# Kernel optimization log

Hardware: AMD Instinct MI355X
Metric: run time of the kernel (lower is better)

The kernel has to match this reference:

```python
import jax, jax.numpy as jnp
import numpy as np

N = 100000  # nodes
E = 1600000  # edges
F_IN = 512
H = 128
C = 40
L = 8
ALPHA = 0.1
THETA = 0.5


def setup_inputs() -> dict:
    key = jax.random.key(0)
    ks = jax.random.split(key, 8)
    x = jax.random.normal(ks[0], (N, F_IN), dtype=jnp.float32)
    edge_index = jax.random.randint(ks[1], (2, E), 0, N, dtype=jnp.int32)
    edge_weight = jax.random.uniform(ks[2], (E,), dtype=jnp.float32)
    W0 = jax.random.normal(ks[3], (F_IN, H), dtype=jnp.float32) * 0.05
    b0 = jnp.zeros((H,), dtype=jnp.float32)
    convW = jax.random.normal(ks[4], (L, H, H), dtype=jnp.float32) * 0.05
    W1 = jax.random.normal(ks[5], (H, C), dtype=jnp.float32) * 0.05
    b1 = jnp.zeros((C,), dtype=jnp.float32)
    return {"x": x, "edge_index": edge_index, "edge_weight": edge_weight,
            "W0": W0, "b0": b0, "convW": convW, "W1": W1, "b1": b1}


def reference(x, edge_index, edge_weight, W0, b0, convW, W1, b1):
    # eval mode, dropout=0.0 -> dropout is identity
    src, dst = edge_index[0], edge_index[1]
    h = jnp.maximum(x @ W0 + b0, 0.0)  # [N, H]
    x0 = h  # initial residual
    # GCN2Conv beta per layer: log(theta/layer + 1), layer = 1..L
    betas = jnp.log(THETA / jnp.arange(1, L + 1, dtype=jnp.float32) + 1.0)

    def layer(h, inputs):
        W, beta = inputs  # W: [H, H]
        # sparse adjacency propagation: sum_j A_ij * h_j
        msgs = h[src] * edge_weight[:, None]  # [E, H]
        agg = jax.ops.segment_sum(msgs, dst, num_segments=N)  # [N, H]
        # initial residual mixing + identity mapping (shared_weights=True)
        out = (1.0 - ALPHA) * agg + ALPHA * x0
        out = (1.0 - beta) * out + beta * (out @ W)
        return jnp.maximum(out, 0.0), None

    h, _ = jax.lax.scan(layer, h, (convW, betas))
    logits = h @ W1 + b1  # [N, C]
    return jax.nn.log_softmax(logits, axis=-1)
```

## Files before the change

### kernel.cpp

```cpp
#include <hip/hip_runtime.h>
#include <hip/hip_bf16.h>
#include <cmath>

#define NN 100000
#define NE 1600000
#define FIN 512
#define HD 128
#define NC 40
#define NL 8
#define SCB 512

typedef __attribute__((ext_vector_type(8))) short bh8;
typedef __attribute__((ext_vector_type(4))) float f4;
typedef __attribute__((ext_vector_type(4))) unsigned int u4;
typedef __attribute__((ext_vector_type(2))) unsigned int u2;

__device__ __forceinline__ float bflo(unsigned p){ return __uint_as_float(p << 16); }
__device__ __forceinline__ float bfhi(unsigned p){ return __uint_as_float(p & 0xffff0000u); }
__device__ __forceinline__ unsigned short f2bf(float f){
  unsigned u = __float_as_uint(f);
  u += 0x7fffu + ((u >> 16) & 1u);
  return (unsigned short)(u >> 16);
}
__device__ __forceinline__ unsigned pack2(float a, float b){
  return (unsigned)f2bf(a) | ((unsigned)f2bf(b) << 16);
}

__global__ void k_deg(const int* __restrict__ dst, int* __restrict__ deg, int e){
  for (int i = blockIdx.x * blockDim.x + threadIdx.x; i < e; i += gridDim.x * blockDim.x)
    atomicAdd(&deg[dst[i]], 1);
}

__global__ void k_scan(const int* __restrict__ deg, int* __restrict__ offs,
                       int* __restrict__ cur, int n){
  __shared__ int wsum[16];
  __shared__ int carry;
  int t = threadIdx.x, lane = t & 63, wid = t >> 6;
  if (t == 0) carry = 0;
  __syncthreads();
  for (int base = 0; base < n; base += 1024){
    int idx = base + t;
    int v = (idx < n) ? deg[idx] : 0;
    int orig = v;
    #pragma unroll
    for (int off = 1; off < 64; off <<= 1){
      int u = __shfl_up(v, off);
      if (lane >= off) v += u;
    }
    if (lane == 63) wsum[wid] = v;
    __syncthreads();
    if (wid == 0){
      int s = (lane < 16) ? wsum[lane] : 0;
      #pragma unroll
      for (int off = 1; off < 16; off <<= 1){
        int u = __shfl_up(s, off);
        if (lane >= off) s += u;
      }
      if (lane < 16) wsum[lane] = s;
    }
    __syncthreads();
    int wexcl = (wid == 0) ? 0 : wsum[wid - 1];
    int excl = carry + wexcl + (v - orig);
    if (idx < n){ offs[idx] = excl; cur[idx] = excl; }
    int ctot = wsum[15];
    __syncthreads();
    if (t == 0) carry += ctot;
    __syncthreads();
  }
  if (t == 0) offs[n] = carry;
}

__global__ void k_twt(const float* __restrict__ in, unsigned short* __restrict__ out,
                      int K, int C, int Cpad){
  int total = Cpad * K;
  for (int i = blockIdx.x * blockDim.x + threadIdx.x; i < total; i += gridDim.x * blockDim.x){
    int c = i / K, k = i % K;
    float v = (c < C) ? in[(size_t)k * C + c] : 0.f;
    out[i] = f2bf(v);
  }
}

__global__ __launch_bounds__(256) void k_g0sc(const float* __restrict__ X,
                                              const unsigned short* __restrict__ Wt,
                                              const float* __restrict__ b0,
                                              unsigned* __restrict__ Ha,
                                              unsigned* __restrict__ Hb, int n,
                                              const int* __restrict__ src,
                                              const int* __restrict__ dst,
                                              const float* __restrict__ wgt,
                                              int* __restrict__ cur,
                                              u2* __restrict__ epk, int e){
  __shared__ __attribute__((aligned(16))) char lds[33792];
  if ((int)blockIdx.x < SCB){
    int stride = SCB * 256;
    int i = blockIdx.x * 256 + threadIdx.x;
    for (; i + 3 * stride < e; i += 4 * stride){
      int i0 = i, i1 = i + stride, i2 = i + 2 * stride, i3 = i + 3 * stride;
      int d0 = dst[i0], d1 = dst[i1], d2 = dst[i2], d3 = dst[i3];
      int p0 = atomicAdd(&cur[d0], 1);
      int p1 = atomicAdd(&cur[d1], 1);
      int p2 = atomicAdd(&cur[d2], 1);
      int p3 = atomicAdd(&cur[d3], 1);
      u2 v0 = { (unsigned)src[i0], __float_as_uint(wgt[i0]) };
      u2 v1 = { (unsigned)src[i1], __float_as_uint(wgt[i1]) };
      u2 v2 = { (unsigned)src[i2], __float_as_uint(wgt[i2]) };
      u2 v3 = { (unsigned)src[i3], __float_as_uint(wgt[i3]) };
      epk[p0] = v0; epk[p1] = v1; epk[p2] = v2; epk[p3] = v3;
    }
    for (; i < e; i += stride){
      int d = dst[i];
      int p = atomicAdd(&cur[d], 1);
      u2 v = { (unsigned)src[i], __float_as_uint(wgt[i]) };
      epk[p] = v;
    }
    return;
  }
  char* ldsA = lds;
  char* ldsW = lds + 8192;
  float* ldsO = (float*)lds;
  int t = threadIdx.x;
  int w = t >> 6, lane = t & 63;
  int rowBase = (blockIdx.x - SCB) * 64;
  f4 acc[8];
  #pragma unroll
  for (int i = 0; i < 8; i++) acc[i] = (f4)0.f;

  for (int kk = 0; kk < 8; kk++){
    #pragma unroll
    for (int iter = 0; iter < 2; iter++){
      int r = t / 8 + iter * 32;
      int kc = (t % 8) * 8;
      int grow = rowBase + r;
      float4 f0 = {0,0,0,0}, f1 = {0,0,0,0};
      if (grow < n){
        const float4* p = (const float4*)(X + (size_t)grow * FIN + kk * 64 + kc);
        f0 = p[0]; f1 = p[1];
      }
      u4 pv = { pack2(f0.x, f0.y), pack2(f0.z, f0.w), pack2(f1.x, f1.y), pack2(f1.z, f1.w) };
      *(u4*)(ldsA + r * 128 + ((kc * 2) ^ ((r & 7) << 4))) = pv;
    }
    #pragma unroll
    for (int iter = 0; iter < 4; iter++){
      int c = t / 8 + iter * 32;
      int kc = (t % 8) * 8;
      bh8 v = *(const bh8*)(Wt + (size_t)c * FIN + kk * 64 + kc);
      *(bh8*)(ldsW + c * 128 + ((kc * 2) ^ ((c & 7) << 4))) = v;
    }
    __syncthreads();
    int rowf = (w << 4) + (lane & 15);
    #pragma unroll
    for (int ks = 0; ks < 2; ks++){
      bh8 fa = *(const bh8*)(ldsA + rowf * 128 + ((ks * 64 + (lane >> 4) * 16) ^ ((rowf & 7) << 4)));
      #pragma unroll
      for (int ct = 0; ct < 8; ct++){
        int colf = (ct << 4) + (lane & 15);
        bh8 fb = *(const bh8*)(ldsW + colf * 128 + ((ks * 64 + (lane >> 4) * 16) ^ ((colf & 7) << 4)));
        acc[ct] = __builtin_amdgcn_mfma_f32_16x16x32_bf16(fa, fb, acc[ct], 0, 0, 0);
      }
    }
    __syncthreads();
  }
  #pragma unroll
  for (int ct = 0; ct < 8; ct++){
    int colf = (ct << 4) + (lane & 15);
    float bb = b0[colf];
    #pragma unroll
    for (int i = 0; i < 4; i++){
      int r = (w << 4) + ((lane >> 4) << 2) + i;
      float v = acc[ct][i] + bb;
      ldsO[r * 132 + colf] = v > 0.f ? v : 0.f;
    }
  }
  __syncthreads();
  #pragma unroll
  for (int iter = 0; iter < 4; iter++){
    int r = iter * 16 + t / 16;
    int c8 = (t % 16) * 8;
    int grow = rowBase + r;
    if (grow < n){
      float* p = &ldsO[r * 132 + c8];
      u4 pv = { pack2(p[0], p[1]), pack2(p[2], p[3]), pack2(p[4], p[5]), pack2(p[6], p[7]) };
      *(u4*)(Ha + (size_t)grow * 64 + (t % 16) * 4) = pv;
      *(u4*)(Hb + (size_t)grow * 64 + (t % 16) * 4) = pv;
    }
  }
}

__global__ __launch_bounds__(512) void k_layer(const unsigned* __restrict__ Hin,
                                               const unsigned* __restrict__ X0,
                                               const int* __restrict__ offs,
                                               const u2* __restrict__ epk,
                                               const unsigned short* __restrict__ Wt,
                                               float beta,
                                               unsigned* __restrict__ Hout, int n){
  __shared__ __attribute__((aligned(16))) char ldsA[16384];
  int t = threadIdx.x;
  int w = t >> 6, lane = t & 63;
  int q = lane >> 4, l16 = lane & 15;
  int quadId = (w << 2) + q;
  int rowBase = blockIdx.x * 64;

  #pragma unroll
  for (int rr = 0; rr < 2; rr++){
    int lr = (quadId << 1) + rr;
    int d = rowBase + lr;
    bool act = d < n;
    int e0 = act ? offs[d] : 0;
    int e1 = act ? offs[d + 1] : 0;
    float a0=0.f,a1=0.f,a2=0.f,a3=0.f,a4=0.f,a5=0.f,a6=0.f,a7=0.f;
    int e = e0;
    for (; e + 7 < e1; e += 8){
      #pragma unroll
      for (int j = 0; j < 8; j++){
        u2 pe = epk[e + j];
        float wf = __uint_as_float(pe.y);
        u4 r = *(const u4*)(Hin + (size_t)pe.x * 64 + l16 * 4);
        a0 += wf * bflo(r.x); a1 += wf * bfhi(r.x);
        a2 += wf * bflo(r.y); a3 += wf * bfhi(r.y);
        a4 += wf * bflo(r.z); a5 += wf * bfhi(r.z);
        a6 += wf * bflo(r.w); a7 += wf * bfhi(r.w);
      }
    }
    for (; e < e1; e++){
      u2 pe = epk[e];
      float wf = __uint_as_float(pe.y);
      u4 r = *(const u4*)(Hin + (size_t)pe.x * 64 + l16 * 4);
      a0 += wf * bflo(r.x); a1 += wf * bfhi(r.x);
      a2 += wf * bflo(r.y); a3 += wf * bfhi(r.y);
      a4 += wf * bflo(r.z); a5 += wf * bfhi(r.z);
      a6 += wf * bflo(r.w); a7 += wf * bfhi(r.w);
    }
    u4 ov = { 0u, 0u, 0u, 0u };
    if (act){
      u4 xp = *(const u4*)(X0 + (size_t)d * 64 + l16 * 4);
      float v0 = 0.9f*a0 + 0.1f*bflo(xp.x), v1 = 0.9f*a1 + 0.1f*bfhi(xp.x);
      float v2 = 0.9f*a2 + 0.1f*bflo(xp.y), v3 = 0.9f*a3 + 0.1f*bfhi(xp.y);
      float v4 = 0.9f*a4 + 0.1f*bflo(xp.z), v5 = 0.9f*a5 + 0.1f*bfhi(xp.z);
      float v6 = 0.9f*a6 + 0.1f*bflo(xp.w), v7 = 0.9f*a7 + 0.1f*bfhi(xp.w);
      ov = (u4){ pack2(v0,v1), pack2(v2,v3), pack2(v4,v5), pack2(v6,v7) };
    }
    *(u4*)(ldsA + lr * 256 + ((l16 * 16) ^ ((lr & 7) << 4))) = ov;
  }
  __syncthreads();

  f4 acc[4];
  #pragma unroll
  for (int i = 0; i < 4; i++) acc[i] = (f4)0.f;
  int rowf = ((w & 3) << 4) + l16;
  int colBase = (w >> 2) << 6;
  #pragma unroll
  for (int ks = 0; ks < 4; ks++){
    bh8 fa = *(const bh8*)(ldsA + rowf * 256 + ((ks * 64 + q * 16) ^ ((rowf & 7) << 4)));
    #pragma unroll
    for (int ct = 0; ct < 4; ct++){
      int colf = colBase + (ct << 4) + l16;
      bh8 fb = *(const bh8*)(Wt + (size_t)colf * HD + ks * 32 + q * 8);
      acc[ct] = __builtin_amdgcn_mfma_f32_16x16x32_bf16(fa, fb, acc[ct], 0, 0, 0);
    }
  }

  #pragma unroll
  for (int ct = 0; ct < 4; ct++){
    int colf = colBase + (ct << 4) + l16;
    #pragma unroll
    for (int i = 0; i < 4; i++){
      int r = ((w & 3) << 4) + (q << 2) + i;
      char* addr = ldsA + r * 256 + ((colf * 2) ^ ((r & 7) << 4));
      unsigned short tv = *(const unsigned short*)addr;
      float tf = __uint_as_float(((unsigned)tv) << 16);
      float v = (1.f - beta) * tf + beta * acc[ct][i];
      *(unsigned short*)addr = f2bf(v > 0.f ? v : 0.f);
    }
  }
  __syncthreads();

  #pragma unroll
  for (int iter = 0; iter < 2; iter++){
    int r = iter * 32 + t / 16;
    int kc = (t % 16) * 8;
    int grow = rowBase + r;
    if (grow < n){
      bh8 v = *(const bh8*)(ldsA + r * 256 + ((kc * 2) ^ ((r & 7) << 4)));
      *(bh8*)((unsigned short*)Hout + (size_t)grow * HD + kc) = v;
    }
  }
}

__global__ __launch_bounds__(256) void k_final(const unsigned* __restrict__ H,
                                               const unsigned short* __restrict__ W1t,
                                               const float* __restrict__ b1,
                                               float* __restrict__ out, int n){
  __shared__ __attribute__((aligned(16))) char lds[16384 + 12288];
  char* ldsA = lds;
  char* ldsW = lds + 16384;
  int t = threadIdx.x;
  int w = t >> 6, lane = t & 63;
  int l15 = lane & 15;
  int rowBase = blockIdx.x * 64;
  const unsigned short* Hs = (const unsigned short*)H;

  #pragma unroll
  for (int iter = 0; iter < 4; iter++){
    int r = t / 16 + iter * 16;
    int kc = (t % 16) * 8;
    int grow = rowBase + r;
    bh8 v = (bh8)(short)0;
    if (grow < n) v = *(const bh8*)(Hs + (size_t)grow * HD + kc);
    *(bh8*)(ldsA + r * 256 + ((kc * 2) ^ ((r & 7) << 4))) = v;
  }
  #pragma unroll
  for (int iter = 0; iter < 3; iter++){
    int c = t / 16 + iter * 16;
    int kc = (t % 16) * 8;
    bh8 v = *(const bh8*)(W1t + (size_t)c * HD + kc);
    *(bh8*)(ldsW + c * 256 + ((kc * 2) ^ ((c & 7) << 4))) = v;
  }
  __syncthreads();

  f4 acc[3];
  #pragma unroll
  for (int i = 0; i < 3; i++) acc[i] = (f4)0.f;
  int rowf = (w << 4) + l15;
  #pragma unroll
  for (int ks = 0; ks < 4; ks++){
    bh8 fa = *(const bh8*)(ldsA + rowf * 256 + ((ks * 64 + (lane >> 4) * 16) ^ ((rowf & 7) << 4)));
    #pragma unroll
    for (int ct = 0; ct < 3; ct++){
      int colf = (ct << 4) + l15;
      bh8 fb = *(const bh8*)(ldsW + colf * 256 + ((ks * 64 + (lane >> 4) * 16) ^ ((colf & 7) << 4)));
      acc[ct] = __builtin_amdgcn_mfma_f32_16x16x32_bf16(fa, fb, acc[ct], 0, 0, 0);
    }
  }

  float bias0 = b1[l15];
  float bias1 = b1[16 + l15];
  bool v2ok = (l15 < 8);
  float bias2 = v2ok ? b1[32 + l15] : 0.f;

  #pragma unroll
  for (int i = 0; i < 4; i++){
    int r = rowBase + (w << 4) + ((lane >> 4) << 2) + i;
    float v0 = acc[0][i] + bias0;
    float v1 = acc[1][i] + bias1;
    float v2 = v2ok ? (acc[2][i] + bias2) : -1e30f;
    float m = fmaxf(fmaxf(v0, v1), v2);
    #pragma unroll
    for (int off = 1; off < 16; off <<= 1) m = fmaxf(m, __shfl_xor(m, off));
    float e0 = __expf(v0 - m), e1 = __expf(v1 - m);
    float e2 = v2ok ? __expf(v2 - m) : 0.f;
    float s = e0 + e1 + e2;
    #pragma unroll
    for (int off = 1; off < 16; off <<= 1) s += __shfl_xor(s, off);
    float ls = m + __logf(s);
    if (r < n){
      out[(size_t)r * NC + l15] = v0 - ls;
      out[(size_t)r * NC + 16 + l15] = v1 - ls;
      if (v2ok) out[(size_t)r * NC + 32 + l15] = v2 - ls;
    }
  }
}

extern "C" void kernel_launch(void* const* d_in, const int* in_sizes, int n_in,
                              void* d_out, int out_size, void* d_ws, size_t ws_size,
                              hipStream_t stream){
  const float* x  = (const float*)d_in[0];
  const int*   ei = (const int*)d_in[1];
  const float* ew = (const float*)d_in[2];
  const float* W0 = (const float*)d_in[3];
  const float* b0 = (const float*)d_in[4];
  const float* cW = (const float*)d_in[5];
  const float* W1 = (const float*)d_in[6];
  const float* b1 = (const float*)d_in[7];
  float* out = (float*)d_out;
  const int* src = ei;
  const int* dst = ei + NE;

  char* ws = (char*)d_ws;
  size_t off = 0;
  auto alloc = [&](size_t bytes) -> char* {
    char* p = ws + off;
    off += (bytes + 255) & ~(size_t)255;
    return p;
  };
  unsigned* x0b = (unsigned*)alloc((size_t)NN * 64 * 4);
  unsigned* hbA = (unsigned*)alloc((size_t)NN * 64 * 4);
  unsigned* hbB = (unsigned*)alloc((size_t)NN * 64 * 4);
  unsigned short* W0t = (unsigned short*)alloc((size_t)FIN * HD * 2);
  unsigned short* cWt = (unsigned short*)alloc((size_t)NL * HD * HD * 2);
  unsigned short* W1t = (unsigned short*)alloc((size_t)48 * HD * 2);
  int*   deg  = (int*)alloc((size_t)NN * 4);
  int*   offs = (int*)alloc((size_t)(NN + 1) * 4);
  int*   cur  = (int*)alloc((size_t)NN * 4);
  u2*    epk  = (u2*)alloc((size_t)NE * 8);

  (void)hipMemsetAsync(deg, 0, (size_t)NN * 4, stream);
  hipLaunchKernelGGL(k_deg, dim3(2048), dim3(256), 0, stream, dst, deg, NE);
  hipLaunchKernelGGL(k_scan, dim3(1), dim3(1024), 0, stream, deg, offs, cur, NN);
  hipLaunchKernelGGL(k_twt, dim3(256), dim3(256), 0, stream, W0, W0t, FIN, HD, HD);
  for (int l = 0; l < NL; l++)
    hipLaunchKernelGGL(k_twt, dim3(64), dim3(256), 0, stream,
                       cW + (size_t)l * HD * HD, cWt + (size_t)l * HD * HD, HD, HD, HD);
  hipLaunchKernelGGL(k_twt, dim3(24), dim3(256), 0, stream, W1, W1t, HD, NC, 48);

  int gblocks = (NN + 63) / 64;
  hipLaunchKernelGGL(k_g0sc, dim3(SCB + gblocks), dim3(256), 0, stream,
                     x, W0t, b0, x0b, hbA, NN, src, dst, ew, cur, epk, NE);
  for (int l = 0; l < NL; l++){
    float beta = logf(0.5f / (float)(l + 1) + 1.0f);
    const unsigned* hin = (l & 1) ? hbB : hbA;
    unsigned* hout = (l & 1) ? hbA : hbB;
    hipLaunchKernelGGL(k_layer, dim3(gblocks), dim3(512), 0, stream,
                       hin, x0b, offs, epk, cWt + (size_t)l * HD * HD, beta, hout, NN);
  }
  hipLaunchKernelGGL(k_final, dim3(gblocks), dim3(256), 0, stream, hbA, W1t, b1, out, NN);
}
```

Baseline: 1.173 ms.

## Build CSR via two-level bucket partition instead of global atomic scatter

Replaces the degree-count, single-block 100k scan and global-atomic scatter into CSR with a two-pass radix-style partition. Edges are first bucketed by dst>>9 into 196 coarse buckets using LDS histograms, then each bucket is locally sorted in LDS to produce offsets and the final packed edge list. The intent is to cut the global atomic contention and the serial scan cost. It also merges the eleven weight-transpose launches into one, and drops the overlap of the scatter with the first GEMM, adding an extra temporary edge buffer pass. Edges within a node keep a nondeterministic order, as before.

```diff
diff --git a/kernel.cpp b/kernel.cpp
--- a/kernel.cpp
+++ b/kernel.cpp
@@ -8,7 +8,9 @@
 #define HD 128
 #define NC 40
 #define NL 8
-#define SCB 512
+#define NBK 196
+#define P1B 256
+#define CHUNK ((NE + P1B - 1) / P1B)
 
 typedef __attribute__((ext_vector_type(8))) short bh8;
 typedef __attribute__((ext_vector_type(4))) float f4;
@@ -26,101 +28,148 @@
   return (unsigned)f2bf(a) | ((unsigned)f2bf(b) << 16);
 }
 
-__global__ void k_deg(const int* __restrict__ dst, int* __restrict__ deg, int e){
-  for (int i = blockIdx.x * blockDim.x + threadIdx.x; i < e; i += gridDim.x * blockDim.x)
-    atomicAdd(&deg[dst[i]], 1);
-}
-
-__global__ void k_scan(const int* __restrict__ deg, int* __restrict__ offs,
-                       int* __restrict__ cur, int n){
-  __shared__ int wsum[16];
-  __shared__ int carry;
-  int t = threadIdx.x, lane = t & 63, wid = t >> 6;
-  if (t == 0) carry = 0;
-  __syncthreads();
-  for (int base = 0; base < n; base += 1024){
-    int idx = base + t;
-    int v = (idx < n) ? deg[idx] : 0;
+__global__ __launch_bounds__(256) void k_hist(const int* __restrict__ dst,
+                                              int* __restrict__ bcnt){
+  __shared__ int h[256];
+  int t = threadIdx.x;
+  h[t] = 0;
+  __syncthreads();
+  int lo = blockIdx.x * CHUNK;
+  int hi = lo + CHUNK < NE ? lo + CHUNK : NE;
+  for (int i = lo + t; i < hi; i += 256)
+    atomicAdd(&h[dst[i] >> 9], 1);
+  __syncthreads();
+  if (h[t]) atomicAdd(&bcnt[t], h[t]);
+}
+
+__global__ void k_bscan(const int* __restrict__ bcnt, int* __restrict__ gbase,
+                        int* __restrict__ gcur, int* __restrict__ offs){
+  int t = threadIdx.x;
+  int carry = 0;
+  for (int base = 0; base < 256; base += 64){
+    int v = bcnt[base + t];
     int orig = v;
     #pragma unroll
     for (int off = 1; off < 64; off <<= 1){
       int u = __shfl_up(v, off);
-      if (lane >= off) v += u;
-    }
-    if (lane == 63) wsum[wid] = v;
-    __syncthreads();
-    if (wid == 0){
-      int s = (lane < 16) ? wsum[lane] : 0;
+      if (t >= off) v += u;
+    }
+    int excl = carry + v - orig;
+    gbase[base + t] = excl;
+    gcur[base + t] = excl;
+    carry += __shfl(v, 63);
+  }
+  if (t == 0){ gbase[256] = carry; offs[NN] = NE; }
+}
+
+__global__ __launch_bounds__(256) void k_part(const int* __restrict__ src,
+                                              const int* __restrict__ dst,
+                                              const float* __restrict__ w,
+                                              int* __restrict__ gcur,
+                                              u2* __restrict__ tmp){
+  __shared__ int h[256];
+  __shared__ int base[256];
+  int t = threadIdx.x;
+  h[t] = 0;
+  __syncthreads();
+  int lo = blockIdx.x * CHUNK;
+  int hi = lo + CHUNK < NE ? lo + CHUNK : NE;
+  for (int i = lo + t; i < hi; i += 256)
+    atomicAdd(&h[dst[i] >> 9], 1);
+  __syncthreads();
+  int cnt = h[t];
+  if (cnt) base[t] = atomicAdd(&gcur[t], cnt);
+  h[t] = 0;
+  __syncthreads();
+  for (int i = lo + t; i < hi; i += 256){
+    int d = dst[i];
+    int bk = d >> 9;
+    int r = atomicAdd(&h[bk], 1);
+    u2 v = { (unsigned)src[i] | ((unsigned)(d & 511) << 17), __float_as_uint(w[i]) };
+    tmp[base[bk] + r] = v;
+  }
+}
+
+__global__ __launch_bounds__(256) void k_place(const u2* __restrict__ tmp,
+                                               const int* __restrict__ gbase,
+                                               int* __restrict__ offs,
+                                               u2* __restrict__ epk){
+  __shared__ int h[512];
+  __shared__ int lofs[512];
+  int b = blockIdx.x;
+  int t = threadIdx.x;
+  int e0 = gbase[b], e1 = gbase[b + 1];
+  h[t] = 0; h[t + 256] = 0;
+  __syncthreads();
+  for (int i = e0 + t; i < e1; i += 256)
+    atomicAdd(&h[tmp[i].x >> 17], 1);
+  __syncthreads();
+  if (t < 64){
+    int carry = 0;
+    for (int base = 0; base < 512; base += 64){
+      int v = h[base + t];
+      int orig = v;
       #pragma unroll
-      for (int off = 1; off < 16; off <<= 1){
-        int u = __shfl_up(s, off);
-        if (lane >= off) s += u;
+      for (int off = 1; off < 64; off <<= 1){
+        int u = __shfl_up(v, off);
+        if (t >= off) v += u;
       }
-      if (lane < 16) wsum[lane] = s;
-    }
-    __syncthreads();
-    int wexcl = (wid == 0) ? 0 : wsum[wid - 1];
-    int excl = carry + wexcl + (v - orig);
-    if (idx < n){ offs[idx] = excl; cur[idx] = excl; }
-    int ctot = wsum[15];
-    __syncthreads();
-    if (t == 0) carry += ctot;
-    __syncthreads();
-  }
-  if (t == 0) offs[n] = carry;
-}
-
-__global__ void k_twt(const float* __restrict__ in, unsigned short* __restrict__ out,
-                      int K, int C, int Cpad){
-  int total = Cpad * K;
+      lofs[base + t] = carry + v - orig;
+      carry += __shfl(v, 63);
+    }
+  }
+  __syncthreads();
+  int d = b * 512 + t;
+  if (d < NN) offs[d] = e0 + lofs[t];
+  int d2 = b * 512 + 256 + t;
+  if (d2 < NN) offs[d2] = e0 + lofs[256 + t];
+  h[t] = 0; h[t + 256] = 0;
+  __syncthreads();
+  for (int i = e0 + t; i < e1; i += 256){
+    u2 v = tmp[i];
+    int d9 = v.x >> 17;
+    int r = atomicAdd(&h[d9], 1);
+    u2 o = { v.x & 0x1FFFFu, v.y };
+    epk[e0 + lofs[d9] + r] = o;
+  }
+}
+
+__global__ void k_twt_all(const float* __restrict__ W0, const float* __restrict__ cW,
+                          const float* __restrict__ W1, unsigned short* __restrict__ out){
+  const int n0 = FIN * HD;
+  const int n1 = NL * HD * HD;
+  const int total = n0 + n1 + 48 * HD;
   for (int i = blockIdx.x * blockDim.x + threadIdx.x; i < total; i += gridDim.x * blockDim.x){
-    int c = i / K, k = i % K;
-    float v = (c < C) ? in[(size_t)k * C + c] : 0.f;
+    float v;
+    if (i < n0){
+      int c = i / FIN, k = i % FIN;
+      v = W0[(size_t)k * HD + c];
+    } else if (i < n0 + n1){
+      int j = i - n0;
+      int l = j / (HD * HD), r = j % (HD * HD);
+      int c = r / HD, k = r % HD;
+      v = cW[(size_t)l * HD * HD + k * HD + c];
+    } else {
+      int j = i - n0 - n1;
+      int c = j / HD, k = j % HD;
+      v = (c < NC) ? W1[(size_t)k * NC + c] : 0.f;
+    }
     out[i] = f2bf(v);
   }
 }
 
-__global__ __launch_bounds__(256) void k_g0sc(const float* __restrict__ X,
-                                              const unsigned short* __restrict__ Wt,
-                                              const float* __restrict__ b0,
-                                              unsigned* __restrict__ Ha,
-                                              unsigned* __restrict__ Hb, int n,
-                                              const int* __restrict__ src,
-                                              const int* __restrict__ dst,
-                                              const float* __restrict__ wgt,
-                                              int* __restrict__ cur,
-                                              u2* __restrict__ epk, int e){
+__global__ __launch_bounds__(256) void k_gemm0(const float* __restrict__ X,
+                                               const unsigned short* __restrict__ Wt,
+                                               const float* __restrict__ b0,
+                                               unsigned* __restrict__ Ha,
+                                               unsigned* __restrict__ Hb, int n){
   __shared__ __attribute__((aligned(16))) char lds[33792];
-  if ((int)blockIdx.x < SCB){
-    int stride = SCB * 256;
-    int i = blockIdx.x * 256 + threadIdx.x;
-    for (; i + 3 * stride < e; i += 4 * stride){
-      int i0 = i, i1 = i + stride, i2 = i + 2 * stride, i3 = i + 3 * stride;
-      int d0 = dst[i0], d1 = dst[i1], d2 = dst[i2], d3 = dst[i3];
-      int p0 = atomicAdd(&cur[d0], 1);
-      int p1 = atomicAdd(&cur[d1], 1);
-      int p2 = atomicAdd(&cur[d2], 1);
-      int p3 = atomicAdd(&cur[d3], 1);
-      u2 v0 = { (unsigned)src[i0], __float_as_uint(wgt[i0]) };
-      u2 v1 = { (unsigned)src[i1], __float_as_uint(wgt[i1]) };
-      u2 v2 = { (unsigned)src[i2], __float_as_uint(wgt[i2]) };
-      u2 v3 = { (unsigned)src[i3], __float_as_uint(wgt[i3]) };
-      epk[p0] = v0; epk[p1] = v1; epk[p2] = v2; epk[p3] = v3;
-    }
-    for (; i < e; i += stride){
-      int d = dst[i];
-      int p = atomicAdd(&cur[d], 1);
-      u2 v = { (unsigned)src[i], __float_as_uint(wgt[i]) };
-      epk[p] = v;
-    }
-    return;
-  }
   char* ldsA = lds;
   char* ldsW = lds + 8192;
   float* ldsO = (float*)lds;
   int t = threadIdx.x;
   int w = t >> 6, lane = t & 63;
-  int rowBase = (blockIdx.x - SCB) * 64;
+  int rowBase = blockIdx.x * 64;
   f4 acc[8];
   #pragma unroll
   for (int i = 0; i < 8; i++) acc[i] = (f4)0.f;
@@ -385,26 +434,26 @@
   unsigned* x0b = (unsigned*)alloc((size_t)NN * 64 * 4);
   unsigned* hbA = (unsigned*)alloc((size_t)NN * 64 * 4);
   unsigned* hbB = (unsigned*)alloc((size_t)NN * 64 * 4);
-  unsigned short* W0t = (unsigned short*)alloc((size_t)FIN * HD * 2);
-  unsigned short* cWt = (unsigned short*)alloc((size_t)NL * HD * HD * 2);
-  unsigned short* W1t = (unsigned short*)alloc((size_t)48 * HD * 2);
-  int*   deg  = (int*)alloc((size_t)NN * 4);
-  int*   offs = (int*)alloc((size_t)(NN + 1) * 4);
-  int*   cur  = (int*)alloc((size_t)NN * 4);
-  u2*    epk  = (u2*)alloc((size_t)NE * 8);
-
-  (void)hipMemsetAsync(deg, 0, (size_t)NN * 4, stream);
-  hipLaunchKernelGGL(k_deg, dim3(2048), dim3(256), 0, stream, dst, deg, NE);
-  hipLaunchKernelGGL(k_scan, dim3(1), dim3(1024), 0, stream, deg, offs, cur, NN);
-  hipLaunchKernelGGL(k_twt, dim3(256), dim3(256), 0, stream, W0, W0t, FIN, HD, HD);
-  for (int l = 0; l < NL; l++)
-    hipLaunchKernelGGL(k_twt, dim3(64), dim3(256), 0, stream,
-                       cW + (size_t)l * HD * HD, cWt + (size_t)l * HD * HD, HD, HD, HD);
-  hipLaunchKernelGGL(k_twt, dim3(24), dim3(256), 0, stream, W1, W1t, HD, NC, 48);
+  unsigned short* wbuf = (unsigned short*)alloc(((size_t)FIN * HD + (size_t)NL * HD * HD + 48 * HD) * 2);
+  unsigned short* W0t = wbuf;
+  unsigned short* cWt = wbuf + (size_t)FIN * HD;
+  unsigned short* W1t = cWt + (size_t)NL * HD * HD;
+  int*   offs  = (int*)alloc((size_t)(NN + 1) * 4);
+  int*   bcnt  = (int*)alloc(256 * 4);
+  int*   gbase = (int*)alloc(257 * 4);
+  int*   gcur  = (int*)alloc(256 * 4);
+  u2*    tmp   = (u2*)alloc((size_t)NE * 8);
+  u2*    epk   = (u2*)alloc((size_t)NE * 8);
+
+  (void)hipMemsetAsync(bcnt, 0, 256 * 4, stream);
+  hipLaunchKernelGGL(k_hist, dim3(P1B), dim3(256), 0, stream, dst, bcnt);
+  hipLaunchKernelGGL(k_bscan, dim3(1), dim3(64), 0, stream, bcnt, gbase, gcur, offs);
+  hipLaunchKernelGGL(k_part, dim3(P1B), dim3(256), 0, stream, src, dst, ew, gcur, tmp);
+  hipLaunchKernelGGL(k_place, dim3(NBK), dim3(256), 0, stream, tmp, gbase, offs, epk);
+  hipLaunchKernelGGL(k_twt_all, dim3(256), dim3(256), 0, stream, W0, cW, W1, wbuf);
 
   int gblocks = (NN + 63) / 64;
-  hipLaunchKernelGGL(k_g0sc, dim3(SCB + gblocks), dim3(256), 0, stream,
-                     x, W0t, b0, x0b, hbA, NN, src, dst, ew, cur, epk, NE);
+  hipLaunchKernelGGL(k_gemm0, dim3(gblocks), dim3(256), 0, stream, x, W0t, b0, x0b, hbA, NN);
   for (int l = 0; l < NL; l++){
     float beta = logf(0.5f / (float)(l + 1) + 1.0f);
     const unsigned* hin = (l & 1) ? hbB : hbA;
```

Result: faster. 1.000 ms (-14.7%).
